# Kernel tuning notes

Hardware: AMD Instinct MI355X
Metric: run time of the kernel (lower is better)

## Reference

```python
import jax, jax.numpy as jnp
import numpy as np

D = 512
NH = 8
DH = D // NH
B, L = 16, 1024


def setup_inputs() -> dict:
    key = jax.random.key(0)
    k1, k2, k3, k4 = jax.random.split(key, 4)
    queries = jax.random.normal(k1, (B, D, L), dtype=jnp.float32)
    mask = jax.random.randint(k2, (B, L), 0, 2, dtype=jnp.int32)
    # xavier-ish scale for 1x1 conv weights [out, in]
    w_mem = jax.random.normal(k3, (2 * D, D), dtype=jnp.float32) * (1.0 / np.sqrt(D))
    w_q = jax.random.normal(k4, (D, D), dtype=jnp.float32) * (1.0 / np.sqrt(D))
    return {"queries": queries, "mask": mask, "w_mem": w_mem, "w_q": w_q}


def _split_heads(x):
    # [B, L, D] -> [B, NH, L, DH]
    b, l, _ = x.shape
    return x.reshape(b, l, NH, DH).transpose(0, 2, 1, 3)


def reference(queries, mask, w_mem, w_q):
    # queries: [B, D, L] channels-first (1x1 Conv1d == per-position matmul)
    x = queries.transpose(0, 2, 1)                       # [B, L, D]
    mem = jnp.einsum('bld,ed->ble', x, w_mem)            # [B, L, 2D]
    qry = jnp.einsum('bld,ed->ble', x, w_q)              # [B, L, D]
    q = _split_heads(qry) * (DH ** -0.5)                 # [B, NH, L, DH]
    k = _split_heads(mem[..., :D])
    v = _split_heads(mem[..., D:])
    logits = jnp.einsum('bhqd,bhkd->bhqk', q, k)         # [B, NH, L, L]
    maskf = mask.astype(jnp.float32)[:, None, None, :]   # [B,1,1,L]
    logits = logits + (-1e30) * (1.0 - maskf)
    weights = jax.nn.softmax(logits, axis=-1)
    out = jnp.einsum('bhqk,bhkd->bhqd', weights, v)      # [B, NH, L, DH]
    out = out.transpose(0, 2, 1, 3).reshape(B, L, D)     # combine heads
    return out.transpose(0, 2, 1)                        # [B, D, L]
```

## Files before the change

### kernel.cpp

```cpp
#include <hip/hip_runtime.h>
#include <hip/hip_bf16.h>
#include <stdint.h>

#define Bsz 16
#define NHn 8
#define Dm  512
#define DHd 64
#define Ls  1024

typedef __attribute__((ext_vector_type(8))) short bf16x8;
typedef __attribute__((ext_vector_type(4))) float f32x4;
typedef __attribute__((ext_vector_type(16))) float f32x16;
typedef __attribute__((ext_vector_type(4))) unsigned int u32x4;

#define MFMA16 __builtin_amdgcn_mfma_f32_16x16x32_bf16
#define MFMA32 __builtin_amdgcn_mfma_f32_32x32x16_bf16

#define QSCALE 0.18033688011112042f

static __device__ __forceinline__ unsigned short f2bf(float f) {
    unsigned int u = __builtin_bit_cast(unsigned int, f);
    u += 0x7FFFu + ((u >> 16) & 1u);
    return (unsigned short)(u >> 16);
}

static __device__ __forceinline__ void gl2lds16(const void* g, void* l) {
    __builtin_amdgcn_global_load_lds(
        (const __attribute__((address_space(1))) unsigned int*)g,
        (__attribute__((address_space(3))) unsigned int*)l, 16, 0, 0);
}

__global__ void __launch_bounds__(256) pack_x(const float* __restrict__ q,
                                              unsigned short* __restrict__ X) {
    __shared__ float tile[64][68];
    const int bid = blockIdx.x;
    const int b  = bid >> 7;
    const int dt = (bid >> 4) & 7;
    const int lt = bid & 15;
    const int t  = threadIdx.x;
    const int tr = t >> 4;
    const int tc = (t & 15) * 4;
    const float* src = q + ((size_t)b * Dm + dt * 64) * Ls + lt * 64;
#pragma unroll
    for (int p = 0; p < 4; ++p) {
        const int r = p * 16 + tr;
        const float4 v = *(const float4*)(src + (size_t)r * Ls + tc);
        tile[r][tc+0] = v.x; tile[r][tc+1] = v.y; tile[r][tc+2] = v.z; tile[r][tc+3] = v.w;
    }
    __syncthreads();
    unsigned short* dst = X + (size_t)(b * Ls + lt * 64) * Dm + dt * 64;
#pragma unroll
    for (int p = 0; p < 4; ++p) {
        const int lr = p * 16 + tr;
        ushort4 o;
        o.x = f2bf(tile[tc+0][lr]);
        o.y = f2bf(tile[tc+1][lr]);
        o.z = f2bf(tile[tc+2][lr]);
        o.w = f2bf(tile[tc+3][lr]);
        *(ushort4*)(dst + (size_t)lr * Dm + tc) = o;
    }
}

__global__ void __launch_bounds__(256) pack_w(const float* __restrict__ wm,
                                              const float* __restrict__ wq,
                                              unsigned short* __restrict__ W) {
    const int i = (blockIdx.x * 256 + threadIdx.x) * 4;
    const int n = i >> 9;
    const int k = i & 511;
    const float* src = (n < 512) ? (wq + (size_t)n * 512 + k)
                                 : (wm + (size_t)(n - 512) * 512 + k);
    const float4 v = *(const float4*)src;
    ushort4 o;
    o.x = f2bf(v.x); o.y = f2bf(v.y); o.z = f2bf(v.z); o.w = f2bf(v.w);
    *(ushort4*)(W + i) = o;
}

__global__ void __launch_bounds__(512) gemm_qkv(const unsigned short* __restrict__ X,
                                                const unsigned short* __restrict__ W,
                                                const int* __restrict__ mask,
                                                unsigned short* __restrict__ Qb,
                                                unsigned short* __restrict__ Kb,
                                                unsigned short* __restrict__ VT) {
    __shared__ unsigned short Alds[2][128 * 64];
    __shared__ unsigned short Blds[2][128 * 64];
    const int bid = (blockIdx.x & 7) * 192 + (blockIdx.x >> 3);
    const int nt = bid % 12, mt = bid / 12;
    const int m0 = mt * 128, n0 = nt * 128;
    const int t = threadIdx.x;
    const int w = t >> 6, lane = t & 63, g = lane >> 4, c = lane & 15;
    const int wm = w >> 1, wn = w & 1;

    const int srow = t >> 3;
    const int scol = (((t & 7) ^ (srow & 7))) * 8;

    f32x4 acc[2][4];
#pragma unroll
    for (int i = 0; i < 2; ++i)
#pragma unroll
        for (int j = 0; j < 4; ++j) acc[i][j] = f32x4{0.f, 0.f, 0.f, 0.f};

#define STAGE(BUF, KT) do {                                                      \
        const int k0_ = (KT) * 64;                                               \
        gl2lds16(X + (size_t)(m0 + srow) * Dm + k0_ + scol,                      \
                 &Alds[BUF][w * 512]);                                           \
        gl2lds16(X + (size_t)(m0 + 64 + srow) * Dm + k0_ + scol,                 \
                 &Alds[BUF][4096 + w * 512]);                                    \
        gl2lds16(W + (size_t)(n0 + srow) * Dm + k0_ + scol,                      \
                 &Blds[BUF][w * 512]);                                           \
        gl2lds16(W + (size_t)(n0 + 64 + srow) * Dm + k0_ + scol,                 \
                 &Blds[BUF][4096 + w * 512]);                                    \
    } while (0)

#define KLOOP(SWAPPED) do {                                                      \
    for (int kt = 0; kt < 8; ++kt) {                                             \
        const int buf = kt & 1;                                                  \
        if (kt < 7) {                                                            \
            STAGE(buf ^ 1, kt + 1);                                              \
            asm volatile("s_waitcnt vmcnt(4)" ::: "memory");                     \
        } else {                                                                 \
            asm volatile("s_waitcnt vmcnt(0)" ::: "memory");                     \
        }                                                                        \
        __syncthreads();                                                         \
        const char* Ab = (const char*)&Alds[buf][0];                             \
        const char* Bb = (const char*)&Blds[buf][0];                             \
        _Pragma("unroll")                                                        \
        for (int kk = 0; kk < 2; ++kk) {                                         \
            bf16x8 av[2], bv[4];                                                 \
            _Pragma("unroll")                                                    \
            for (int mi = 0; mi < 2; ++mi) {                                     \
                const int R = wm * 32 + mi * 16 + c;                             \
                av[mi] = *(const bf16x8*)(Ab + R * 128 +                         \
                          ((kk * 64 + g * 16) ^ ((R & 7) << 4)));                \
            }                                                                    \
            _Pragma("unroll")                                                    \
            for (int nj = 0; nj < 4; ++nj) {                                     \
                const int R = wn * 64 + nj * 16 + c;                             \
                bv[nj] = *(const bf16x8*)(Bb + R * 128 +                         \
                          ((kk * 64 + g * 16) ^ ((R & 7) << 4)));                \
            }                                                                    \
            _Pragma("unroll")                                                    \
            for (int mi = 0; mi < 2; ++mi)                                       \
                _Pragma("unroll")                                                \
                for (int nj = 0; nj < 4; ++nj)                                   \
                    acc[mi][nj] = (SWAPPED)                                      \
                        ? MFMA16(bv[nj], av[mi], acc[mi][nj], 0, 0, 0)           \
                        : MFMA16(av[mi], bv[nj], acc[mi][nj], 0, 0, 0);          \
        }                                                                        \
        __syncthreads();                                                         \
    }                                                                            \
} while (0)

    STAGE(0, 0);
    const int bq = m0 >> 10;

    if (n0 < 1024) {
        KLOOP(1);
        const int m_loc = (m0 & 1023) + wm * 32 + c;
        const int hbase = ((n0 < 512) ? n0 : (n0 - 512)) >> 6;
        const bool isK = (n0 >= 512);
        unsigned short* dstbase = isK ? Kb : Qb;
        const float scale = isK ? 1.0f : QSCALE;
        unsigned short* base = dstbase + ((size_t)(bq * NHn + hbase + wn) * Ls) * DHd;
        const int dh0 = g * 4;
        int mk[2];
#pragma unroll
        for (int mi = 0; mi < 2; ++mi)
            mk[mi] = isK ? mask[bq * Ls + m_loc + mi * 16] : 1;
#pragma unroll
        for (int nj = 0; nj < 4; ++nj) {
#pragma unroll
            for (int mi = 0; mi < 2; ++mi) {
                ushort4 o;
                if (mk[mi]) {
                    o.x = f2bf(acc[mi][nj][0] * scale);
                    o.y = f2bf(acc[mi][nj][1] * scale);
                    o.z = f2bf(acc[mi][nj][2] * scale);
                    o.w = f2bf(acc[mi][nj][3] * scale);
                } else {
                    o.x = 0; o.y = 0; o.z = 0; o.w = 0;
                }
                *(ushort4*)(base + (size_t)(m_loc + mi * 16) * DHd + nj * 16 + dh0) = o;
            }
        }
    } else {
        KLOOP(0);
        const int m_loc = (m0 & 1023) + wm * 32 + g * 4;
        const int hbase = (n0 - 1024) >> 6;
        unsigned short* base = VT + ((size_t)(bq * NHn + hbase + wn) * DHd) * Ls;
        int4 mv[2];
#pragma unroll
        for (int mi = 0; mi < 2; ++mi)
            mv[mi] = *(const int4*)(mask + bq * Ls + m_loc + mi * 16);
#pragma unroll
        for (int nj = 0; nj < 4; ++nj) {
            const int dh = nj * 16 + c;
#pragma unroll
            for (int mi = 0; mi < 2; ++mi) {
                ushort4 o;
                o.x = mv[mi].x ? f2bf(acc[mi][nj][0]) : (unsigned short)0;
                o.y = mv[mi].y ? f2bf(acc[mi][nj][1]) : (unsigned short)0;
                o.z = mv[mi].z ? f2bf(acc[mi][nj][2]) : (unsigned short)0;
                o.w = mv[mi].w ? f2bf(acc[mi][nj][3]) : (unsigned short)0;
                *(ushort4*)(base + (size_t)dh * Ls + m_loc + mi * 16) = o;
            }
        }
    }
#undef KLOOP
#undef STAGE
}

__global__ void __launch_bounds__(512) attn(const unsigned short* __restrict__ Qb,
                                            const unsigned short* __restrict__ Kb,
                                            const unsigned short* __restrict__ VT,
                                            const int* __restrict__ mask,
                                            float* __restrict__ out) {
    __shared__ unsigned short Klds[2][4096];
    __shared__ unsigned short Vlds[2][4096];

    const int bid = blockIdx.x;
    const int xcd = bid & 7;
    const int idx = bid >> 3;
    const int qblk = idx & 3;
    const int bh = ((idx >> 2) << 3) | xcd;
    const int b = bh >> 3, h = bh & 7;
    const int t = threadIdx.x, w = t >> 6, lane = t & 63;
    const int c5 = lane & 31, hi = lane >> 5;
    const int sw = (c5 & 7) << 4;

    const unsigned short* Qh = Qb + (size_t)bh * (Ls * DHd);
    const unsigned short* Kh = Kb + (size_t)bh * (Ls * DHd);
    const unsigned short* Vh = VT + (size_t)bh * (DHd * Ls);
    const int q = qblk * 256 + w * 32 + c5;

    float fnmask;
    {
        int s = 0;
        const int4* mp = (const int4*)(mask + b * Ls);
#pragma unroll
        for (int j = 0; j < 4; ++j) {
            const int4 mv = mp[j * 64 + lane];
            s += (mv.x + mv.y) + (mv.z + mv.w);
        }
#pragma unroll
        for (int off = 1; off < 64; off <<= 1) s += __shfl_xor(s, off);
        fnmask = (float)(Ls - s);
    }

    bf16x8 qf[4];
#pragma unroll
    for (int ks = 0; ks < 4; ++ks)
        qf[ks] = *(const bf16x8*)(Qh + (size_t)q * DHd + ks * 16 + hi * 8);

    const int r0 = t >> 3, c0b = (t & 7) << 4;
    const int ksrc0 = r0 * 128  + (c0b ^ ((r0 & 7) << 4));
    const int vsrc0 = r0 * 2048 + (c0b ^ ((r0 & 7) << 4));

#define STAGE(BUF, KV0) do {                                          \
        const char* Kc = (const char*)Kh + (size_t)(KV0) * 128;       \
        const char* Vc = (const char*)Vh + (size_t)(KV0) * 2;         \
        gl2lds16(Kc + ksrc0, &Klds[BUF][w * 512]);                    \
        gl2lds16(Vc + vsrc0, &Vlds[BUF][w * 512]);                    \
    } while (0)

    STAGE(0, 0);

    float lsum = 0.f;
    f32x16 oacc0, oacc1;
#pragma unroll
    for (int i = 0; i < 16; ++i) { oacc0[i] = 0.f; oacc1[i] = 0.f; }

    for (int it = 0; it < 16; ++it) {
        const int kv0 = it * 64;
        const int buf = it & 1;
        asm volatile("s_waitcnt vmcnt(0)" ::: "memory");
        __syncthreads();
        if (it < 15) STAGE(buf ^ 1, kv0 + 64);

        f32x16 acc0, acc1;
#pragma unroll
        for (int i = 0; i < 16; ++i) { acc0[i] = 0.f; acc1[i] = 0.f; }

        const char* Kbase = (const char*)&Klds[buf][0];
        __builtin_amdgcn_s_setprio(1);
#pragma unroll
        for (int ks = 0; ks < 4; ++ks) {
            const bf16x8 k0 = *(const bf16x8*)(Kbase + c5 * 128 + ((ks * 32 + hi * 16) ^ sw));
            acc0 = MFMA32(k0, qf[ks], acc0, 0, 0, 0);
            const bf16x8 k1 = *(const bf16x8*)(Kbase + (32 + c5) * 128 + ((ks * 32 + hi * 16) ^ sw));
            acc1 = MFMA32(k1, qf[ks], acc1, 0, 0, 0);
        }
        __builtin_amdgcn_s_setprio(0);

        unsigned pk0[8], pk1[8];
#pragma unroll
        for (int u = 0; u < 4; ++u) {
            float p0 = __builtin_amdgcn_exp2f(acc0[4*u+0]);
            float p1 = __builtin_amdgcn_exp2f(acc0[4*u+1]);
            float p2 = __builtin_amdgcn_exp2f(acc0[4*u+2]);
            float p3 = __builtin_amdgcn_exp2f(acc0[4*u+3]);
            lsum += (p0 + p1) + (p2 + p3);
            asm("v_cvt_pk_bf16_f32 %0, %1, %2" : "=v"(pk0[2*u+0]) : "v"(p0), "v"(p1));
            asm("v_cvt_pk_bf16_f32 %0, %1, %2" : "=v"(pk0[2*u+1]) : "v"(p2), "v"(p3));
            float s0 = __builtin_amdgcn_exp2f(acc1[4*u+0]);
            float s1 = __builtin_amdgcn_exp2f(acc1[4*u+1]);
            float s2 = __builtin_amdgcn_exp2f(acc1[4*u+2]);
            float s3 = __builtin_amdgcn_exp2f(acc1[4*u+3]);
            lsum += (s0 + s1) + (s2 + s3);
            asm("v_cvt_pk_bf16_f32 %0, %1, %2" : "=v"(pk1[2*u+0]) : "v"(s0), "v"(s1));
            asm("v_cvt_pk_bf16_f32 %0, %1, %2" : "=v"(pk1[2*u+1]) : "v"(s2), "v"(s3));
        }

        const char* Vbase = (const char*)&Vlds[buf][0];
#define PV_STEP(S, PK) do {                                                         \
            unsigned a0 = PK[2 * (2 * ((S) & 1) + 0) + 0];                          \
            unsigned a1 = PK[2 * (2 * ((S) & 1) + 0) + 1];                          \
            unsigned b0 = PK[2 * (2 * ((S) & 1) + 1) + 0];                          \
            unsigned b1 = PK[2 * (2 * ((S) & 1) + 1) + 1];                          \
            asm("v_permlane32_swap_b32 %0, %1" : "+v"(a0), "+v"(b0));               \
            asm("v_permlane32_swap_b32 %0, %1" : "+v"(a1), "+v"(b1));               \
            const u32x4 fw = {a0, a1, b0, b1};                                      \
            const bf16x8 pf = __builtin_bit_cast(bf16x8, fw);                       \
            const bf16x8 v0 = *(const bf16x8*)(Vbase + c5 * 128 + (((S) * 32 + hi * 16) ^ sw)); \
            oacc0 = MFMA32(v0, pf, oacc0, 0, 0, 0);                                 \
            const bf16x8 v1 = *(const bf16x8*)(Vbase + (32 + c5) * 128 + (((S) * 32 + hi * 16) ^ sw)); \
            oacc1 = MFMA32(v1, pf, oacc1, 0, 0, 0);                                 \
        } while (0)
        __builtin_amdgcn_s_setprio(1);
        PV_STEP(0, pk0);
        PV_STEP(1, pk0);
        PV_STEP(2, pk1);
        PV_STEP(3, pk1);
        __builtin_amdgcn_s_setprio(0);
#undef PV_STEP
    }

    lsum += __shfl_xor(lsum, 32);
    lsum -= fnmask;
    const float rinv = __builtin_amdgcn_rcpf(lsum);
    float* ob = out + (size_t)(b * Dm + h * DHd) * Ls + q;
#pragma unroll
    for (int reg = 0; reg < 16; ++reg) {
        const int dh = (reg & 3) + 8 * (reg >> 2) + 4 * hi;
        ob[(size_t)dh * Ls] = oacc0[reg] * rinv;
    }
#pragma unroll
    for (int reg = 0; reg < 16; ++reg) {
        const int dh = 32 + (reg & 3) + 8 * (reg >> 2) + 4 * hi;
        ob[(size_t)dh * Ls] = oacc1[reg] * rinv;
    }
#undef STAGE
}

extern "C" void kernel_launch(void* const* d_in, const int* in_sizes, int n_in,
                              void* d_out, int out_size, void* d_ws, size_t ws_size,
                              hipStream_t stream) {
    const float* queries = (const float*)d_in[0];
    const int*   mask    = (const int*)d_in[1];
    const float* w_mem   = (const float*)d_in[2];
    const float* w_q     = (const float*)d_in[3];
    float* out = (float*)d_out;

    char* ws = (char*)d_ws;
    unsigned short* X  = (unsigned short*)(ws);
    unsigned short* W  = (unsigned short*)(ws + 16777216);
    unsigned short* Qb = (unsigned short*)(ws + 18350080);
    unsigned short* Kb = (unsigned short*)(ws + 35127296);
    unsigned short* VT = (unsigned short*)(ws + 51904512);
    if (ws_size < 68681728) return;

    pack_x<<<dim3(2048), dim3(256), 0, stream>>>(queries, X);
    pack_w<<<dim3(768),  dim3(256), 0, stream>>>(w_mem, w_q, W);
    gemm_qkv<<<dim3(1536), dim3(512), 0, stream>>>(X, W, mask, Qb, Kb, VT);
    attn<<<dim3(512), dim3(512), 0, stream>>>(Qb, Kb, VT, mask, out);
}
```

Baseline: 90.10 us.

## Merge pack kernels and have each GEMM block compute two N-tiles

Fuses the activation and weight bf16 packing kernels into one launch, which removes a kernel launch and its inter-kernel gap. The QKV GEMM now launches half as many blocks, and each block processes two 128-wide N tiles in sequence for the same M tile. The aim is to improve A-tile reuse in L2 and cut block scheduling overhead. The cost is less parallelism and a serialized second tile per block, with an explicit vmcnt wait between the two passes.

```diff
diff --git a/kernel.cpp b/kernel.cpp
--- a/kernel.cpp
+++ b/kernel.cpp
@@ -30,49 +30,50 @@
         (__attribute__((address_space(3))) unsigned int*)l, 16, 0, 0);
 }
 
-__global__ void __launch_bounds__(256) pack_x(const float* __restrict__ q,
-                                              unsigned short* __restrict__ X) {
+__global__ void __launch_bounds__(256) pack_xw(const float* __restrict__ q,
+                                               const float* __restrict__ wm,
+                                               const float* __restrict__ wq,
+                                               unsigned short* __restrict__ X,
+                                               unsigned short* __restrict__ W) {
     __shared__ float tile[64][68];
-    const int bid = blockIdx.x;
-    const int b  = bid >> 7;
-    const int dt = (bid >> 4) & 7;
-    const int lt = bid & 15;
-    const int t  = threadIdx.x;
-    const int tr = t >> 4;
-    const int tc = (t & 15) * 4;
-    const float* src = q + ((size_t)b * Dm + dt * 64) * Ls + lt * 64;
-#pragma unroll
-    for (int p = 0; p < 4; ++p) {
-        const int r = p * 16 + tr;
-        const float4 v = *(const float4*)(src + (size_t)r * Ls + tc);
-        tile[r][tc+0] = v.x; tile[r][tc+1] = v.y; tile[r][tc+2] = v.z; tile[r][tc+3] = v.w;
-    }
-    __syncthreads();
-    unsigned short* dst = X + (size_t)(b * Ls + lt * 64) * Dm + dt * 64;
-#pragma unroll
-    for (int p = 0; p < 4; ++p) {
-        const int lr = p * 16 + tr;
+    const int t = threadIdx.x;
+    if (blockIdx.x < 2048) {
+        const int bid = blockIdx.x;
+        const int b  = bid >> 7;
+        const int dt = (bid >> 4) & 7;
+        const int lt = bid & 15;
+        const int tr = t >> 4;
+        const int tc = (t & 15) * 4;
+        const float* src = q + ((size_t)b * Dm + dt * 64) * Ls + lt * 64;
+#pragma unroll
+        for (int p = 0; p < 4; ++p) {
+            const int r = p * 16 + tr;
+            const float4 v = *(const float4*)(src + (size_t)r * Ls + tc);
+            tile[r][tc+0] = v.x; tile[r][tc+1] = v.y; tile[r][tc+2] = v.z; tile[r][tc+3] = v.w;
+        }
+        __syncthreads();
+        unsigned short* dst = X + (size_t)(b * Ls + lt * 64) * Dm + dt * 64;
+#pragma unroll
+        for (int p = 0; p < 4; ++p) {
+            const int lr = p * 16 + tr;
+            ushort4 o;
+            o.x = f2bf(tile[tc+0][lr]);
+            o.y = f2bf(tile[tc+1][lr]);
+            o.z = f2bf(tile[tc+2][lr]);
+            o.w = f2bf(tile[tc+3][lr]);
+            *(ushort4*)(dst + (size_t)lr * Dm + tc) = o;
+        }
+    } else {
+        const int i = ((blockIdx.x - 2048) * 256 + t) * 4;
+        const int n = i >> 9;
+        const int k = i & 511;
+        const float* src = (n < 512) ? (wq + (size_t)n * 512 + k)
+                                     : (wm + (size_t)(n - 512) * 512 + k);
+        const float4 v = *(const float4*)src;
         ushort4 o;
-        o.x = f2bf(tile[tc+0][lr]);
-        o.y = f2bf(tile[tc+1][lr]);
-        o.z = f2bf(tile[tc+2][lr]);
-        o.w = f2bf(tile[tc+3][lr]);
-        *(ushort4*)(dst + (size_t)lr * Dm + tc) = o;
-    }
-}
-
-__global__ void __launch_bounds__(256) pack_w(const float* __restrict__ wm,
-                                              const float* __restrict__ wq,
-                                              unsigned short* __restrict__ W) {
-    const int i = (blockIdx.x * 256 + threadIdx.x) * 4;
-    const int n = i >> 9;
-    const int k = i & 511;
-    const float* src = (n < 512) ? (wq + (size_t)n * 512 + k)
-                                 : (wm + (size_t)(n - 512) * 512 + k);
-    const float4 v = *(const float4*)src;
-    ushort4 o;
-    o.x = f2bf(v.x); o.y = f2bf(v.y); o.z = f2bf(v.z); o.w = f2bf(v.w);
-    *(ushort4*)(W + i) = o;
+        o.x = f2bf(v.x); o.y = f2bf(v.y); o.z = f2bf(v.z); o.w = f2bf(v.w);
+        *(ushort4*)(W + i) = o;
+    }
 }
 
 __global__ void __launch_bounds__(512) gemm_qkv(const unsigned short* __restrict__ X,
@@ -83,9 +84,9 @@
                                                 unsigned short* __restrict__ VT) {
     __shared__ unsigned short Alds[2][128 * 64];
     __shared__ unsigned short Blds[2][128 * 64];
-    const int bid = (blockIdx.x & 7) * 192 + (blockIdx.x >> 3);
-    const int nt = bid % 12, mt = bid / 12;
-    const int m0 = mt * 128, n0 = nt * 128;
+    const int bid = (blockIdx.x & 7) * 96 + (blockIdx.x >> 3);
+    const int pc = bid % 6, mt = bid / 6;
+    const int m0 = mt * 128;
     const int t = threadIdx.x;
     const int w = t >> 6, lane = t & 63, g = lane >> 4, c = lane & 15;
     const int wm = w >> 1, wn = w & 1;
@@ -93,11 +94,8 @@
     const int srow = t >> 3;
     const int scol = (((t & 7) ^ (srow & 7))) * 8;
 
+    int n0;
     f32x4 acc[2][4];
-#pragma unroll
-    for (int i = 0; i < 2; ++i)
-#pragma unroll
-        for (int j = 0; j < 4; ++j) acc[i][j] = f32x4{0.f, 0.f, 0.f, 0.f};
 
 #define STAGE(BUF, KT) do {                                                      \
         const int k0_ = (KT) * 64;                                               \
@@ -150,61 +148,96 @@
     }                                                                            \
 } while (0)
 
-    STAGE(0, 0);
+#define ACC_RESET() do {                                                         \
+        _Pragma("unroll")                                                        \
+        for (int i_ = 0; i_ < 2; ++i_)                                           \
+            _Pragma("unroll")                                                    \
+            for (int j_ = 0; j_ < 4; ++j_)                                       \
+                acc[i_][j_] = f32x4{0.f, 0.f, 0.f, 0.f};                         \
+    } while (0)
+
     const int bq = m0 >> 10;
 
-    if (n0 < 1024) {
-        KLOOP(1);
-        const int m_loc = (m0 & 1023) + wm * 32 + c;
-        const int hbase = ((n0 < 512) ? n0 : (n0 - 512)) >> 6;
-        const bool isK = (n0 >= 512);
-        unsigned short* dstbase = isK ? Kb : Qb;
-        const float scale = isK ? 1.0f : QSCALE;
-        unsigned short* base = dstbase + ((size_t)(bq * NHn + hbase + wn) * Ls) * DHd;
-        const int dh0 = g * 4;
-        int mk[2];
-#pragma unroll
-        for (int mi = 0; mi < 2; ++mi)
-            mk[mi] = isK ? mask[bq * Ls + m_loc + mi * 16] : 1;
-#pragma unroll
-        for (int nj = 0; nj < 4; ++nj) {
-#pragma unroll
-            for (int mi = 0; mi < 2; ++mi) {
-                ushort4 o;
-                if (mk[mi]) {
-                    o.x = f2bf(acc[mi][nj][0] * scale);
-                    o.y = f2bf(acc[mi][nj][1] * scale);
-                    o.z = f2bf(acc[mi][nj][2] * scale);
-                    o.w = f2bf(acc[mi][nj][3] * scale);
-                } else {
-                    o.x = 0; o.y = 0; o.z = 0; o.w = 0;
-                }
-                *(ushort4*)(base + (size_t)(m_loc + mi * 16) * DHd + nj * 16 + dh0) = o;
-            }
+#define EPI_QK() do {                                                            \
+        const int m_loc = (m0 & 1023) + wm * 32 + c;                             \
+        const int hbase = ((n0 < 512) ? n0 : (n0 - 512)) >> 6;                   \
+        const bool isK = (n0 >= 512);                                            \
+        unsigned short* dstbase = isK ? Kb : Qb;                                 \
+        const float scale = isK ? 1.0f : QSCALE;                                 \
+        unsigned short* base = dstbase +                                         \
+            ((size_t)(bq * NHn + hbase + wn) * Ls) * DHd;                        \
+        const int dh0 = g * 4;                                                   \
+        int mk[2];                                                               \
+        _Pragma("unroll")                                                        \
+        for (int mi = 0; mi < 2; ++mi)                                           \
+            mk[mi] = isK ? mask[bq * Ls + m_loc + mi * 16] : 1;                  \
+        _Pragma("unroll")                                                        \
+        for (int nj = 0; nj < 4; ++nj) {                                         \
+            _Pragma("unroll")                                                    \
+            for (int mi = 0; mi < 2; ++mi) {                                     \
+                ushort4 o;                                                       \
+                if (mk[mi]) {                                                    \
+                    o.x = f2bf(acc[mi][nj][0] * scale);                          \
+                    o.y = f2bf(acc[mi][nj][1] * scale);                          \
+                    o.z = f2bf(acc[mi][nj][2] * scale);                          \
+                    o.w = f2bf(acc[mi][nj][3] * scale);                          \
+                } else {                                                         \
+                    o.x = 0; o.y = 0; o.z = 0; o.w = 0;                          \
+                }                                                                \
+                *(ushort4*)(base + (size_t)(m_loc + mi * 16) * DHd               \
+                            + nj * 16 + dh0) = o;                                \
+            }                                                                    \
+        }                                                                        \
+    } while (0)
+
+#define EPI_V() do {                                                             \
+        const int m_loc = (m0 & 1023) + wm * 32 + g * 4;                         \
+        const int hbase = (n0 - 1024) >> 6;                                      \
+        unsigned short* base = VT +                                              \
+            ((size_t)(bq * NHn + hbase + wn) * DHd) * Ls;                        \
+        int4 mv[2];                                                              \
+        _Pragma("unroll")                                                        \
+        for (int mi = 0; mi < 2; ++mi)                                           \
+            mv[mi] = *(const int4*)(mask + bq * Ls + m_loc + mi * 16);           \
+        _Pragma("unroll")                                                        \
+        for (int nj = 0; nj < 4; ++nj) {                                         \
+            const int dh = nj * 16 + c;                                          \
+            _Pragma("unroll")                                                    \
+            for (int mi = 0; mi < 2; ++mi) {                                     \
+                ushort4 o;                                                       \
+                o.x = mv[mi].x ? f2bf(acc[mi][nj][0]) : (unsigned short)0;       \
+                o.y = mv[mi].y ? f2bf(acc[mi][nj][1]) : (unsigned short)0;       \
+                o.z = mv[mi].z ? f2bf(acc[mi][nj][2]) : (unsigned short)0;       \
+                o.w = mv[mi].w ? f2bf(acc[mi][nj][3]) : (unsigned short)0;       \
+                *(ushort4*)(base + (size_t)dh * Ls + m_loc + mi * 16) = o;       \
+            }                                                                    \
+        }                                                                        \
+    } while (0)
+
+    if (pc < 4) {
+#pragma unroll
+        for (int s = 0; s < 2; ++s) {
+            n0 = (pc + 4 * s) * 128;
+            ACC_RESET();
+            STAGE(0, 0);
+            KLOOP(1);
+            EPI_QK();
+            if (s == 0) { asm volatile("s_waitcnt vmcnt(0)" ::: "memory"); }
         }
     } else {
-        KLOOP(0);
-        const int m_loc = (m0 & 1023) + wm * 32 + g * 4;
-        const int hbase = (n0 - 1024) >> 6;
-        unsigned short* base = VT + ((size_t)(bq * NHn + hbase + wn) * DHd) * Ls;
-        int4 mv[2];
-#pragma unroll
-        for (int mi = 0; mi < 2; ++mi)
-            mv[mi] = *(const int4*)(mask + bq * Ls + m_loc + mi * 16);
-#pragma unroll
-        for (int nj = 0; nj < 4; ++nj) {
-            const int dh = nj * 16 + c;
-#pragma unroll
-            for (int mi = 0; mi < 2; ++mi) {
-                ushort4 o;
-                o.x = mv[mi].x ? f2bf(acc[mi][nj][0]) : (unsigned short)0;
-                o.y = mv[mi].y ? f2bf(acc[mi][nj][1]) : (unsigned short)0;
-                o.z = mv[mi].z ? f2bf(acc[mi][nj][2]) : (unsigned short)0;
-                o.w = mv[mi].w ? f2bf(acc[mi][nj][3]) : (unsigned short)0;
-                *(ushort4*)(base + (size_t)dh * Ls + m_loc + mi * 16) = o;
-            }
-        }
-    }
+#pragma unroll
+        for (int s = 0; s < 2; ++s) {
+            n0 = (4 + pc + 2 * s) * 128;
+            ACC_RESET();
+            STAGE(0, 0);
+            KLOOP(0);
+            EPI_V();
+            if (s == 0) { asm volatile("s_waitcnt vmcnt(0)" ::: "memory"); }
+        }
+    }
+#undef EPI_V
+#undef EPI_QK
+#undef ACC_RESET
 #undef KLOOP
 #undef STAGE
 }
@@ -368,8 +401,7 @@
     unsigned short* VT = (unsigned short*)(ws + 51904512);
     if (ws_size < 68681728) return;
 
-    pack_x<<<dim3(2048), dim3(256), 0, stream>>>(queries, X);
-    pack_w<<<dim3(768),  dim3(256), 0, stream>>>(w_mem, w_q, W);
-    gemm_qkv<<<dim3(1536), dim3(512), 0, stream>>>(X, W, mask, Qb, Kb, VT);
+    pack_xw<<<dim3(2816), dim3(256), 0, stream>>>(queries, w_mem, w_q, X, W);
+    gemm_qkv<<<dim3(768), dim3(512), 0, stream>>>(X, W, mask, Qb, Kb, VT);
     attn<<<dim3(512), dim3(512), 0, stream>>>(Qb, Kb, VT, mask, out);
 }
```

Result: no change. 91.15 us (+1.2%).
